# Kernel optimization log

Hardware: AMD Instinct MI355X
Metric: run time of the kernel (lower is better)

## Reference

```python
import jax, jax.numpy as jnp
import numpy as np

NB = 8          # num_bins
HID = 128       # hidden channels of coupling ResidualNet
TB = 3.0        # tail_bound
MINB = 1e-3     # min bin width / height
MIND = 1e-3     # min derivative
DCONST = float(np.log(np.exp(1.0 - MIND) - 1.0))  # softplus(DCONST)+MIND == 1
LU_EPS = 1e-3


def rqs_inverse(x, uw, uh, ud):
    """Inverse monotonic rational-quadratic spline with linear tails (nflows math).
    x: [B,F]; uw,uh broadcastable to [B,F,NB]; ud broadcastable to [B,F,NB-1]."""
    K = NB
    uw = jnp.broadcast_to(uw, x.shape + (K,))
    uh = jnp.broadcast_to(uh, x.shape + (K,))
    ud = jnp.broadcast_to(ud, x.shape + (K - 1,))
    ud = jnp.pad(ud, [(0, 0)] * x.ndim + [(1, 1)], constant_values=DCONST)  # boundary derivs = 1
    inside = (x >= -TB) & (x <= TB)
    xi = jnp.clip(x, -TB, TB)

    def knots(u):
        v = MINB + (1.0 - MINB * K) * jax.nn.softmax(u, -1)
        c = jnp.concatenate([jnp.zeros(x.shape + (1,), x.dtype), jnp.cumsum(v, -1)], -1)
        c = 2.0 * TB * c - TB
        c = c.at[..., 0].set(-TB).at[..., -1].set(TB)
        return c, c[..., 1:] - c[..., :-1]

    cw, w = knots(uw)   # x-knots / bin widths
    ch, h = knots(uh)   # y-knots / bin heights
    d = MIND + jax.nn.softplus(ud)  # [B,F,K+1] knot derivatives

    # searchsorted on cumheights (inverse direction)
    locs = ch.at[..., -1].add(1e-6)
    idx = jnp.clip(jnp.sum((xi[..., None] >= locs).astype(jnp.int32), -1) - 1, 0, K - 1)[..., None]
    g = lambda a: jnp.take_along_axis(a, idx, -1)[..., 0]
    in_cw, in_w, in_ch, in_h = g(cw), g(w), g(ch), g(h)
    delta = in_h / in_w
    d0 = g(d)
    d1 = jnp.take_along_axis(d, idx + 1, -1)[..., 0]

    t = xi - in_ch
    s = d0 + d1 - 2.0 * delta
    a = t * s + in_h * (delta - d0)
    b = in_h * d0 - t * s
    c = -delta * t
    root = (2.0 * c) / (-b - jnp.sqrt(b * b - 4.0 * a * c))
    out = root * in_w + in_cw
    tm = root * (1.0 - root)
    den = delta + s * tm
    dnum = delta ** 2 * (d1 * root ** 2 + 2.0 * delta * tm + d0 * (1.0 - root) ** 2)
    ld = -(jnp.log(dnum) - 2.0 * jnp.log(den))
    return jnp.where(inside, out, x), jnp.where(inside, ld, 0.0)


def resnet(x, Wi, bi, Wb, bb, Wo, bo):
    # nflows ResidualNet: initial linear, 2 pre-activation residual blocks, final linear
    t = x @ Wi + bi
    for j in range(2):
        r = jax.nn.relu(t) @ Wb[2 * j] + bb[2 * j]
        r = jax.nn.relu(r) @ Wb[2 * j + 1] + bb[2 * j + 1]
        t = t + r
    return t @ Wo + bo


def coupling_inverse(z, Wi, bi, Wb, bb, Wo, bo, uw_u, uh_u, ud_u):
    # alternating mask: even dims = identity split, odd dims = transform split
    ident, trans = z[:, 0::2], z[:, 1::2]
    # unconditional spline on identity features is inverted FIRST, then feeds the net
    ident, ld_u = rqs_inverse(ident, uw_u, uh_u, ud_u)
    B, F = trans.shape
    p = resnet(ident, Wi, bi, Wb, bb, Wo, bo).reshape(B, F, 3 * NB - 1)
    scale = 1.0 / np.sqrt(HID)  # nflows divides widths/heights by sqrt(hidden_features)
    trans, ld_t = rqs_inverse(trans, p[..., :NB] * scale, p[..., NB:2 * NB] * scale, p[..., 2 * NB:])
    out = jnp.stack([ident, trans], -1).reshape(B, -1)
    return out, jnp.sum(ld_u, -1) + jnp.sum(ld_t, -1)


def log_prob(x, loc, log_scale, Wi, bi, Wb, bb, Wo, bo, uw_u, uh_u, ud_u,
             lu_lower, lu_upper, lu_ud, lu_b, perms):
    N, T, D = x.shape
    z = x.reshape(-1, D)
    lq = jnp.zeros((z.shape[0],), x.dtype)
    for i in (2, 1, 0):  # flows = [C0,LU0,C1,LU1,C2,LU2]; invert in reverse order
        # LULinearPermute.inverse: permute, then y = L(Ux) + b, logdet = sum log diag(U)
        zp = z[:, perms[i]]
        diag = jax.nn.softplus(lu_ud[i]) + LU_EPS
        U = jnp.triu(lu_upper[i], 1) + jnp.diag(diag)
        L = jnp.tril(lu_lower[i], -1) + jnp.eye(D, dtype=x.dtype)
        z = (zp @ U.T) @ L.T + lu_b[i]
        lq = lq + jnp.sum(jnp.log(diag))
        z, ld = coupling_inverse(z, Wi[i], bi[i], Wb[i], bb[i], Wo[i], bo[i],
                                 uw_u[i], uh_u[i], ud_u[i])
        lq = lq + ld
    # DiagGaussian base log-prob
    lq = lq - 0.5 * D * jnp.log(2.0 * jnp.pi) \
            - jnp.sum(log_scale + 0.5 * ((z - loc) / jnp.exp(log_scale)) ** 2, -1)
    return lq.reshape(N, T)


def setup_inputs():
    key = jax.random.key(0)
    ks = jax.random.split(key, 16)
    N, T, D, F = 8, 512, 550, 275
    OUT = F * (3 * NB - 1)
    s = 0.1
    return {
        "x": jax.random.normal(ks[0], (N, T, D), jnp.float32),
        "loc": 0.1 * jax.random.normal(ks[1], (D,), jnp.float32),
        "log_scale": jnp.zeros((D,), jnp.float32),
        "Wi": s * jax.random.normal(ks[2], (3, F, HID), jnp.float32),
        "bi": jnp.zeros((3, HID), jnp.float32),
        "Wb": s * jax.random.normal(ks[3], (3, 4, HID, HID), jnp.float32),
        "bb": jnp.zeros((3, 4, HID), jnp.float32),
        "Wo": 0.01 * jax.random.normal(ks[4], (3, HID, OUT), jnp.float32),
        "bo": 0.01 * jax.random.normal(ks[5], (3, OUT), jnp.float32),
        "uw_u": jax.random.uniform(ks[6], (3, F, NB), jnp.float32),
        "uh_u": jax.random.uniform(ks[7], (3, F, NB), jnp.float32),
        "ud_u": jax.random.uniform(ks[8], (3, F, NB - 1), jnp.float32),
        "lu_lower": 0.05 * jax.random.normal(ks[9], (3, D, D), jnp.float32),
        "lu_upper": 0.05 * jax.random.normal(ks[10], (3, D, D), jnp.float32),
        "lu_ud": jnp.full((3, D), DCONST, jnp.float32),
        "lu_b": jnp.zeros((3, D), jnp.float32),
        "perms": jnp.stack([jax.random.permutation(ks[11 + i], D) for i in range(3)]).astype(jnp.int32),
    }


def reference(x, loc, log_scale, Wi, bi, Wb, bb, Wo, bo, uw_u, uh_u, ud_u,
              lu_lower, lu_upper, lu_ud, lu_b, perms):
    # log_prob(x).reshape(N, T); calculate_likelihood would just apply exp/nan->0/clamp on top.
    return log_prob(x, loc, log_scale, Wi, bi, Wb, bb, Wo, bo, uw_u, uh_u, ud_u,
                    lu_lower, lu_upper, lu_ud, lu_b, perms)
```

## Files before the change

### kernel.cpp

```cpp
#include <hip/hip_runtime.h>


#define D_DIM 550
#define D_PAD 576
#define N_PAD_A 640
#define F_DIM 275
#define F_PAD 320
#define FP_HALF 288
#define HID_DIM 128
#define OUT_DIM 6325
#define OUT_PAD 6400
#define FT_PAD 276
#define WO2_ROWS (FT_PAD*32)
#define WO_GX (WO2_ROWS/128)
#define B_ROWS 4096
#define NBINS 8
#define TB_C 3.0f
#define MINB_C 0.001f
#define MIND_C 0.001f
#define DCONST_C 0.53974233f
#define LUEPS_C 0.001f
#define RSQRT_HID 0.08838834764831845f

typedef unsigned short ushort_t;
typedef __attribute__((ext_vector_type(8))) short short8;
typedef __attribute__((ext_vector_type(8))) unsigned short ushort8;
typedef __attribute__((ext_vector_type(4))) unsigned short ushort4v;
typedef __attribute__((ext_vector_type(4))) float f32x4;

__device__ __forceinline__ ushort_t f2bf(float f){
    union{float f; unsigned u;} v; v.f = f;
    unsigned r = v.u + 0x7fffu + ((v.u>>16)&1u);
    return (ushort_t)(r>>16);
}
__device__ __forceinline__ float bf2f(ushort_t h){
    union{unsigned u; float f;} v; v.u = ((unsigned)h)<<16;
    return v.f;
}
__device__ __forceinline__ float softplusf(float x){
    return fmaxf(x, 0.f) + __logf(1.f + __expf(-fabsf(x)));
}

__device__ __forceinline__ void knots_from_u(const float* u, float* c, float* w){
    float m = u[0];
#pragma unroll
    for(int k=1;k<NBINS;k++) m = fmaxf(m, u[k]);
    float e[NBINS]; float s = 0.f;
#pragma unroll
    for(int k=0;k<NBINS;k++){ e[k] = __expf(u[k]-m); s += e[k]; }
    float inv = 1.f/s;
    float cum = 0.f;
    c[0] = -TB_C;
#pragma unroll
    for(int k=0;k<NBINS;k++){
        float v = MINB_C + (1.f - MINB_C*(float)NBINS)*e[k]*inv;
        cum += v;
        c[k+1] = 2.f*TB_C*cum - TB_C;
    }
    c[NBINS] = TB_C;
#pragma unroll
    for(int k=0;k<NBINS;k++) w[k] = c[k+1]-c[k];
}

__device__ __forceinline__ void rqs_inv(float x,
                                        const float* cw, const float* w,
                                        const float* ch, const float* h,
                                        const float* d,
                                        float& out, float& ld){
    bool inside = (x >= -TB_C) && (x <= TB_C);
    float xi = fminf(fmaxf(x, -TB_C), TB_C);
    int idx = 0;
#pragma unroll
    for(int j=1;j<NBINS;j++) idx += (xi >= ch[j]) ? 1 : 0;
    float icw=cw[0], iw=w[0], ich=ch[0], ih=h[0], d0=d[0], d1=d[1];
#pragma unroll
    for(int j=1;j<NBINS;j++){
        if(idx==j){ icw=cw[j]; iw=w[j]; ich=ch[j]; ih=h[j]; d0=d[j]; d1=d[j+1]; }
    }
    float delta = ih/iw;
    float t  = xi - ich;
    float s  = d0 + d1 - 2.f*delta;
    float a  = t*s + ih*(delta - d0);
    float b  = ih*d0 - t*s;
    float c  = -delta*t;
    float disc = b*b - 4.f*a*c;
    float root = 2.f*c / (-b - sqrtf(fmaxf(disc, 0.f)));
    float o  = root*iw + icw;
    float tm = root*(1.f-root);
    float den  = delta + s*tm;
    float dnum = delta*delta*(d1*root*root + 2.f*delta*tm + d0*(1.f-root)*(1.f-root));
    float l = 2.f*__logf(den) - __logf(dnum);
    out = inside ? o : x;
    ld  = inside ? l : 0.f;
}


__global__ void build_knots_kernel(const float* __restrict__ uw_u,
                                   const float* __restrict__ uh_u,
                                   const float* __restrict__ ud_u,
                                   float* __restrict__ knots){
    int g = blockIdx.x*blockDim.x + threadIdx.x;
    if(g >= 3*F_DIM) return;
    float* kb = knots + (size_t)g*43;
    float c[9], w[8];
    knots_from_u(uw_u + (size_t)g*8, c, w);
#pragma unroll
    for(int k=0;k<9;k++) kb[k]=c[k];
#pragma unroll
    for(int k=0;k<8;k++) kb[9+k]=w[k];
    knots_from_u(uh_u + (size_t)g*8, c, w);
#pragma unroll
    for(int k=0;k<9;k++) kb[17+k]=c[k];
#pragma unroll
    for(int k=0;k<8;k++) kb[26+k]=w[k];
    float dend = MIND_C + softplusf(DCONST_C);
    kb[34]=dend; kb[42]=dend;
    const float* ud = ud_u + (size_t)g*7;
#pragma unroll
    for(int k=0;k<7;k++) kb[35+k] = MIND_C + softplusf(ud[k]);
}

__global__ void logdiag_kernel(const float* __restrict__ lu_ud, float* __restrict__ outv){
    int tid = threadIdx.x;
    float s = 0.f;
    for(int k=tid; k<3*D_DIM; k+=256) s += __logf(softplusf(lu_ud[k]) + LUEPS_C);
#pragma unroll
    for(int o=32;o>0;o>>=1) s += __shfl_down(s, o);
    __shared__ float sm[4];
    if((tid&63)==0) sm[tid>>6]=s;
    __syncthreads();
    if(tid==0) outv[0] = sm[0]+sm[1]+sm[2]+sm[3];
}

__global__ void build_L_bf16(const float* __restrict__ lower,
                             ushort_t* __restrict__ Lmb){
    int l = blockIdx.z;
    lower += (size_t)l*D_DIM*D_DIM;
    Lmb += (size_t)l*N_PAD_A*D_PAD;
    int k = blockIdx.x*blockDim.x + threadIdx.x;
    int j = blockIdx.y;
    if(k >= D_DIM) return;
    float lv = (j>k) ? lower[(size_t)j*D_DIM+k] : (j==k ? 1.f : 0.f);
    Lmb[(size_t)j*D_PAD+k] = f2bf(lv);
}

__global__ void build_UT_bf16(const float* __restrict__ upper,
                              const float* __restrict__ ud,
                              const int* __restrict__ perm,
                              ushort_t* __restrict__ UpTb){
    int l = blockIdx.z;
    upper += (size_t)l*D_DIM*D_DIM; ud += (size_t)l*D_DIM; perm += (size_t)l*D_DIM;
    UpTb += (size_t)l*N_PAD_A*D_PAD;
    __shared__ float t[32][33];
    int j0 = blockIdx.x*32, k0 = blockIdx.y*32;
    int tx = threadIdx.x, ty = threadIdx.y;
#pragma unroll
    for(int i=0;i<32;i+=8){
        int j = j0+ty+i, k = k0+tx;
        float uv = 0.f;
        if(j<D_DIM && k<D_DIM){
            if(j<k)       uv = upper[(size_t)j*D_DIM+k];
            else if(j==k) uv = softplusf(ud[k]) + LUEPS_C;
        }
        t[ty+i][tx] = uv;
    }
    __syncthreads();
#pragma unroll
    for(int i=0;i<32;i+=8){
        int k = k0+ty+i, j = j0+tx;
        if(k<D_DIM)
            UpTb[(size_t)perm[k]*D_PAD + j] = f2bf(t[tx][ty+i]);
    }
}

__global__ void convert_pad(const float* __restrict__ in, ushort_t* __restrict__ out,
                            int M, int K, int Mpad, int Kpad){
    int idx = blockIdx.x*256 + threadIdx.x;
    if(idx >= Mpad*Kpad) return;
    int r = idx / Kpad, c = idx - r*Kpad;
    float v = (r<M && c<K) ? in[(size_t)r*K+c] : 0.f;
    out[idx] = f2bf(v);
}

template<int REMAP>
__global__ void transpose_convert(const float* __restrict__ in, ushort_t* __restrict__ out,
                                  int K, int N, int Kpad, int Npad, long s_in, long s_out){
    in += (size_t)blockIdx.z*s_in; out += (size_t)blockIdx.z*s_out;
    __shared__ float t[32][33];
    int kb = blockIdx.x*32, nb = blockIdx.y*32;
    int tx = threadIdx.x, ty = threadIdx.y;
#pragma unroll
    for(int i=0;i<32;i+=8){
        int k = kb+ty+i, n = nb+tx;
        t[ty+i][tx] = (k<K && n<N) ? in[(size_t)k*N+n] : 0.f;
    }
    __syncthreads();
#pragma unroll
    for(int i=0;i<32;i+=8){
        int n = nb+ty+i, k = kb+tx;
        if(REMAP){
            if(n < OUT_DIM && k < Kpad){
                int f = n/23, j = n - 23*f;
                out[(size_t)(f*32+j)*Kpad+k] = f2bf(t[tx][ty+i]);
            }
        } else if(n<Npad && k<Kpad){
            out[(size_t)n*Kpad+k] = f2bf(t[tx][ty+i]);
        }
    }
}

__global__ void reorder_bias(const float* __restrict__ bo, float* __restrict__ bo2){
    int idx = blockIdx.x*256 + threadIdx.x;
    if(idx >= 3*OUT_DIM) return;
    int l = idx/OUT_DIM, n = idx%OUT_DIM;
    int f = n/23, j = n - 23*f;
    bo2[(size_t)l*WO2_ROWS + f*32 + j] = bo[idx];
}

template<int OUTBF>
__global__ __launch_bounds__(256)
void gemm_mfma(const ushort_t* __restrict__ A, const ushort_t* __restrict__ Bt,
               const float* __restrict__ bias, void* __restrict__ Cv,
               int M, int N, int Kpad, long sA, long sB, long sC){
    A  += (size_t)blockIdx.z*sA;
    Bt += (size_t)blockIdx.z*sB;
    __shared__ ushort_t As[128][72];
    __shared__ ushort_t Bs[128][72];
    int tid = threadIdx.x;
    int row0 = blockIdx.y*128, col0 = blockIdx.x*128;
    int wave = tid>>6, lane = tid&63;
    int wm = wave&1, wn = wave>>1;
    int lm = lane&15, quad = lane>>4;
    f32x4 acc[4][4] = {};
    for(int k0=0; k0<Kpad; k0+=64){
#pragma unroll
        for(int it=0; it<4; it++){
            int c = tid + it*256;
            int r = c>>3, c8 = (c&7)*8;
            *(ushort8*)&As[r][c8] = *(const ushort8*)(A + (size_t)(row0+r)*Kpad + k0 + c8);
            *(ushort8*)&Bs[r][c8] = *(const ushort8*)(Bt + (size_t)(col0+r)*Kpad + k0 + c8);
        }
        __syncthreads();
#pragma unroll
        for(int ks=0; ks<2; ks++){
            short8 af[4], bfr[4];
#pragma unroll
            for(int i=0;i<4;i++){
                af[i]  = *(const short8*)&As[wm*64 + i*16 + lm][ks*32 + quad*8];
                bfr[i] = *(const short8*)&Bs[wn*64 + i*16 + lm][ks*32 + quad*8];
            }
#pragma unroll
            for(int i=0;i<4;i++)
#pragma unroll
                for(int j=0;j<4;j++)
                    acc[i][j] = __builtin_amdgcn_mfma_f32_16x16x32_bf16(af[i], bfr[j], acc[i][j], 0, 0, 0);
        }
        __syncthreads();
    }
#pragma unroll
    for(int i=0;i<4;i++){
        int rbase = row0 + wm*64 + i*16 + quad*4;
#pragma unroll
        for(int j=0;j<4;j++){
            int gc = col0 + wn*64 + j*16 + lm;
            if(gc >= N) continue;
            float bv = bias[gc];
#pragma unroll
            for(int r=0;r<4;r++){
                int gr = rbase + r;
                float v = acc[i][j][r] + bv;
                if(OUTBF) ((ushort_t*)Cv + (size_t)blockIdx.z*sC)[(size_t)gr*N+gc] = f2bf(v);
                else      ((float*)Cv + (size_t)blockIdx.z*sC)[(size_t)gr*N+gc] = v;
            }
        }
    }
}

__global__ __launch_bounds__(256)
void resnet_fused(const ushort_t* __restrict__ identb,
                  const ushort_t* __restrict__ WiT,
                  const float* __restrict__ bi,
                  const ushort_t* __restrict__ WbT,
                  const float* __restrict__ bb,
                  ushort_t* __restrict__ tb){
    __shared__ ushort_t As2[16][136];
    int tid = threadIdx.x, wave = tid>>6, lane = tid&63;
    int lm = lane&15, quad = lane>>4;
    int r0 = blockIdx.x*16;
    int arow = r0 + lm;
    f32x4 cur[2] = {};
    f32x4 tsv[2];
    for(int k0=0; k0<F_PAD; k0+=64){
        const ushort_t* ap = identb + (size_t)arow*F_PAD + k0 + quad*8;
        short8 af0 = *(const short8*)(ap);
        short8 af1 = *(const short8*)(ap + 32);
#pragma unroll
        for(int jj=0;jj<2;jj++){
            int n = (wave*2+jj)*16 + lm;
            const ushort_t* wp = WiT + (size_t)n*F_PAD + k0 + quad*8;
            short8 b0 = *(const short8*)(wp);
            short8 b1 = *(const short8*)(wp + 32);
            cur[jj] = __builtin_amdgcn_mfma_f32_16x16x32_bf16(af0, b0, cur[jj], 0, 0, 0);
            cur[jj] = __builtin_amdgcn_mfma_f32_16x16x32_bf16(af1, b1, cur[jj], 0, 0, 0);
        }
    }
#pragma unroll
    for(int jj=0;jj<2;jj++){
        float bv = bi[(wave*2+jj)*16 + lm];
#pragma unroll
        for(int r=0;r<4;r++) cur[jj][r] += bv;
        tsv[jj] = cur[jj];
    }
    short8 wA[2][4], wB[2][4];
#pragma unroll
    for(int jj=0;jj<2;jj++){
        int n = (wave*2+jj)*16 + lm;
        const ushort_t* wp = WbT + (size_t)n*128 + quad*8;
#pragma unroll
        for(int ks=0;ks<4;ks++) wA[jj][ks] = *(const short8*)(wp + ks*32);
    }
#pragma unroll
    for(int st=0; st<4; st++){
        __syncthreads();
#pragma unroll
        for(int jj=0;jj<2;jj++)
#pragma unroll
            for(int r=0;r<4;r++)
                As2[quad*4 + r][(wave*2+jj)*16 + lm] = f2bf(fmaxf(cur[jj][r], 0.f));
        if(st < 3){
#pragma unroll
            for(int jj=0;jj<2;jj++){
                int n = (wave*2+jj)*16 + lm;
                const ushort_t* wp = WbT + (size_t)(st+1)*128*128 + (size_t)n*128 + quad*8;
#pragma unroll
                for(int ks=0;ks<4;ks++){
                    if(st & 1) wA[jj][ks] = *(const short8*)(wp + ks*32);
                    else       wB[jj][ks] = *(const short8*)(wp + ks*32);
                }
            }
        }
        __syncthreads();
        short8 af[4];
#pragma unroll
        for(int ks=0;ks<4;ks++) af[ks] = *(const short8*)&As2[lm][ks*32 + quad*8];
        f32x4 acc[2] = {};
#pragma unroll
        for(int ks=0;ks<4;ks++){
#pragma unroll
            for(int jj=0;jj<2;jj++){
                short8 bf = (st & 1) ? wB[jj][ks] : wA[jj][ks];
                acc[jj] = __builtin_amdgcn_mfma_f32_16x16x32_bf16(af[ks], bf, acc[jj], 0, 0, 0);
            }
        }
#pragma unroll
        for(int jj=0;jj<2;jj++){
            float bv = bb[st*128 + (wave*2+jj)*16 + lm];
#pragma unroll
            for(int r=0;r<4;r++) acc[jj][r] += bv;
        }
        if(st==1 || st==3){
#pragma unroll
            for(int jj=0;jj<2;jj++){
#pragma unroll
                for(int r=0;r<4;r++) acc[jj][r] += tsv[jj][r];
                tsv[jj] = acc[jj];
            }
        }
#pragma unroll
        for(int jj=0;jj<2;jj++) cur[jj] = acc[jj];
    }
#pragma unroll
    for(int jj=0;jj<2;jj++)
#pragma unroll
        for(int r=0;r<4;r++)
            tb[(size_t)(r0 + quad*4 + r)*HID_DIM + (wave*2+jj)*16 + lm] = f2bf(cur[jj][r]);
}

__global__ __launch_bounds__(256)
void zodd_transpose(const float* __restrict__ z2, float* __restrict__ z2oddT){
    __shared__ float s[32][65];
    int r0 = blockIdx.x*64, f0 = blockIdx.y*32;
    int tid = threadIdx.x;
    int f = tid & 31, rb = tid >> 5;
#pragma unroll
    for(int rr=0; rr<8; rr++){
        int r = rb + rr*8;
        int fg = f0 + f;
        float v = (fg < F_DIM) ? z2[(size_t)(r0+r)*D_DIM + 2*fg + 1] : 0.f;
        s[f][r] = v;
    }
    __syncthreads();
    int lane = tid & 63, fb = tid >> 6;
#pragma unroll
    for(int ff=0; ff<8; ff++){
        int fo = fb + ff*4;
        z2oddT[(size_t)(f0+fo)*B_ROWS + r0 + lane] = s[fo][lane];
    }
}

__global__ __launch_bounds__(256, 2)
void wo_spline(const ushort_t* __restrict__ tb,
               const ushort_t* __restrict__ Wo2,
               const float* __restrict__ bo2,
               const float* __restrict__ z2oddT,
               ushort_t* __restrict__ zOddT,
               float* __restrict__ ldpart){
    __shared__ __align__(16) char smem[128*133*4];
    __shared__ float ldred[128];
    ushort_t (*As)[72] = (ushort_t(*)[72])smem;
    ushort_t (*Bs)[72] = (ushort_t(*)[72])(smem + 128*72*2);
    float (*P)[133] = (float(*)[133])smem;
    int tid = threadIdx.x;
    int flat = blockIdx.y*WO_GX + blockIdx.x;
    int flat2 = (flat & 7)*(WO_GX*32/8) + (flat >> 3);
    int cbl = flat2 % WO_GX;
    int rbl = flat2 / WO_GX;
    int row0 = rbl*128, col0 = cbl*128;
    int wave = tid>>6, lane = tid&63;
    int wm = wave&1, wn = wave>>1;
    int lm = lane&15, quad = lane>>4;
    f32x4 acc[4][4] = {};
    for(int k0=0; k0<HID_DIM; k0+=64){
#pragma unroll
        for(int it=0; it<4; it++){
            int c = tid + it*256;
            int r = c>>3, c8 = (c&7)*8;
            *(ushort8*)&As[r][c8] = *(const ushort8*)(tb + (size_t)(row0+r)*HID_DIM + k0 + c8);
            *(ushort8*)&Bs[r][c8] = *(const ushort8*)(Wo2 + (size_t)(col0+r)*HID_DIM + k0 + c8);
        }
        __syncthreads();
#pragma unroll
        for(int ks=0; ks<2; ks++){
            short8 af[4], bfr[4];
#pragma unroll
            for(int i=0;i<4;i++){
                af[i]  = *(const short8*)&As[wm*64 + i*16 + lm][ks*32 + quad*8];
                bfr[i] = *(const short8*)&Bs[wn*64 + i*16 + lm][ks*32 + quad*8];
            }
#pragma unroll
            for(int i=0;i<4;i++)
#pragma unroll
                for(int j=0;j<4;j++)
                    acc[i][j] = __builtin_amdgcn_mfma_f32_16x16x32_bf16(af[i], bfr[j], acc[i][j], 0, 0, 0);
        }
        __syncthreads();
    }
#pragma unroll
    for(int j=0;j<4;j++){
        int cl = wn*64 + j*16 + lm;
        float bv = bo2[col0 + cl];
#pragma unroll
        for(int i=0;i<4;i++){
            int rl = wm*64 + i*16 + quad*4;
#pragma unroll
            for(int r=0;r<4;r++) P[rl+r][cl] = acc[i][j][r] + bv;
        }
    }
    __syncthreads();
    int row = tid & 127;
    int fbase = col0 >> 5;
    float ldsum = 0.f;
    const float dend = MIND_C + softplusf(DCONST_C);
#pragma unroll
    for(int e2=0;e2<2;e2++){
        int feat = (tid>>7) + e2*2;
        int fg = fbase + feat;
        if(fg < F_DIM){
            const float* q = &P[row][feat*32];
            float xv = z2oddT[(size_t)fg*B_ROWS + row0 + row];
            bool inside = (xv >= -TB_C) && (xv <= TB_C);
            float xi = fminf(fmaxf(xv, -TB_C), TB_C);
            float eh[8];
            float mh = -1e30f, sh = 0.f;
#pragma unroll
            for(int k=0;k<8;k++){ float u = q[8+k]*RSQRT_HID; eh[k]=u; mh=fmaxf(mh,u); }
#pragma unroll
            for(int k=0;k<8;k++){ eh[k] = __expf(eh[k]-mh); sh += eh[k]; }
            float invh = (1.f - MINB_C*8.f)/sh;
            int idx = 0;
            {
                float cum = 0.f;
#pragma unroll
                for(int k=0;k<7;k++){
                    cum += MINB_C + eh[k]*invh;
                    float ck = 2.f*TB_C*cum - TB_C;
                    idx += (xi >= ck) ? 1 : 0;
                }
            }
            float ich = -TB_C, ihh = 0.f;
            {
                float cum = 0.f, cprev = -TB_C;
#pragma unroll
                for(int k=0;k<8;k++){
                    cum += MINB_C + eh[k]*invh;
                    float ck = (k==7) ? TB_C : (2.f*TB_C*cum - TB_C);
                    if(idx==k){ ich = cprev; ihh = ck - cprev; }
                    cprev = ck;
                }
            }
            float ew[8];
            float mw = -1e30f, sw = 0.f;
#pragma unroll
            for(int k=0;k<8;k++){ float u = q[k]*RSQRT_HID; ew[k]=u; mw=fmaxf(mw,u); }
#pragma unroll
            for(int k=0;k<8;k++){ ew[k] = __expf(ew[k]-mw); sw += ew[k]; }
            float invw = (1.f - MINB_C*8.f)/sw;
            float icw = -TB_C, iww = 0.f;
            {
                float cum = 0.f, cprev = -TB_C;
#pragma unroll
                for(int k=0;k<8;k++){
                    cum += MINB_C + ew[k]*invw;
                    float ck = (k==7) ? TB_C : (2.f*TB_C*cum - TB_C);
                    if(idx==k){ icw = cprev; iww = ck - cprev; }
                    cprev = ck;
                }
            }
            float d0 = (idx==0) ? dend : (MIND_C + softplusf(q[15+idx]));
            float d1 = (idx==7) ? dend : (MIND_C + softplusf(q[16+idx]));
            float delta = ihh/iww;
            float t  = xi - ich;
            float s  = d0 + d1 - 2.f*delta;
            float a  = t*s + ihh*(delta - d0);
            float b  = ihh*d0 - t*s;
            float c  = -delta*t;
            float disc = fmaxf(b*b - 4.f*a*c, 0.f);
            float root = 2.f*c / (-b - sqrtf(disc));
            float o  = root*iww + icw;
            float tm = root*(1.f-root);
            float den  = delta + s*tm;
            float dnum = delta*delta*(d1*root*root + 2.f*delta*tm + d0*(1.f-root)*(1.f-root));
            float l = 2.f*__logf(den) - __logf(dnum);
            zOddT[(size_t)fg*B_ROWS + row0 + row] = f2bf(inside ? o : xv);
            ldsum += inside ? l : 0.f;
        }
    }
    if(tid >= 128) ldred[tid-128] = ldsum;
    __syncthreads();
    if(tid < 128) ldpart[(size_t)cbl*B_ROWS + row0 + tid] = ldsum + ldred[tid];
}

__global__ __launch_bounds__(256)
void interleave_z(const ushort_t* __restrict__ identb,
                  const ushort_t* __restrict__ zOddT,
                  const float* __restrict__ ldpart,
                  ushort_t* __restrict__ znb,
                  float* __restrict__ lq){
    __shared__ ushort_t s[FP_HALF][34];
    int r0 = blockIdx.x*32;
    int tid = threadIdx.x;
#pragma unroll
    for(int i=0;i<36;i++){
        int idx = tid + i*256;
        int f = idx>>5, r = idx&31;
        s[f][r] = zOddT[(size_t)f*B_ROWS + r0 + r];
    }
    __syncthreads();
    int wv = tid>>6, lane = tid&63;
#pragma unroll
    for(int k=0;k<8;k++){
        int r = wv + k*4;
        const ushort_t* idr = identb + (size_t)(r0+r)*F_PAD;
        unsigned* orow = (unsigned*)(znb + (size_t)(r0+r)*D_PAD);
#pragma unroll
        for(int c=0;c<5;c++){
            int f = lane + c*64;
            if(f < FP_HALF){
                unsigned lo = idr[f];
                unsigned hi = s[f][r];
                orow[f] = lo | (hi<<16);
            }
        }
    }
    if(tid < 32){
        float acc = 0.f;
        for(int cb=0; cb<WO_GX; cb++)
            acc += ldpart[(size_t)cb*B_ROWS + r0 + tid];
        lq[r0 + tid] += acc;
    }
}


__global__ __launch_bounds__(320)
void ident_spline_kernel(const float* __restrict__ z2, const float* __restrict__ knots,
                         int layer, ushort_t* __restrict__ identb,
                         float* __restrict__ lq){
    int row = blockIdx.x; int tid = threadIdx.x;
    float ldv = 0.f;
    if(tid < F_DIM){
        const float* kb = knots + ((size_t)(layer*F_DIM + tid))*43;
        float x = z2[(size_t)row*D_DIM + 2*tid];
        float o, l;
        rqs_inv(x, kb, kb+9, kb+17, kb+26, kb+34, o, l);
        identb[(size_t)row*F_PAD + tid] = f2bf(o);
        ldv = l;
    } else {
        identb[(size_t)row*F_PAD + tid] = 0;
    }
    __shared__ float sm[5];
    float v = ldv;
#pragma unroll
    for(int o=32;o>0;o>>=1) v += __shfl_down(v, o);
    if((tid&63)==0) sm[tid>>6]=v;
    __syncthreads();
    if(tid==0) lq[row] += sm[0]+sm[1]+sm[2]+sm[3]+sm[4];
}

__global__ __launch_bounds__(320)
void finalize_kernel(const ushort_t* __restrict__ zb, const float* __restrict__ loc,
                     const float* __restrict__ lsc, const float* __restrict__ lq,
                     const float* __restrict__ logdiag, float* __restrict__ out){
    int row = blockIdx.x; int tid = threadIdx.x;
    float s = 0.f;
    for(int k=tid; k<D_DIM; k+=320){
        float l = lsc[k];
        float diff = (bf2f(zb[(size_t)row*D_PAD+k])-loc[k])*__expf(-l);
        s += l + 0.5f*diff*diff;
    }
    __shared__ float sm[5];
#pragma unroll
    for(int o=32;o>0;o>>=1) s += __shfl_down(s, o);
    if((tid&63)==0) sm[tid>>6]=s;
    __syncthreads();
    if(tid==0){
        float tot = sm[0]+sm[1]+sm[2]+sm[3]+sm[4];
        out[row] = lq[row] + logdiag[0] - 275.f*1.8378770664f - tot;
    }
}


extern "C" void kernel_launch(void* const* d_in, const int* in_sizes, int n_in,
                              void* d_out, int out_size, void* d_ws, size_t ws_size,
                              hipStream_t stream){
    const float* x        = (const float*)d_in[0];
    const float* loc      = (const float*)d_in[1];
    const float* lsc      = (const float*)d_in[2];
    const float* Wi       = (const float*)d_in[3];
    const float* bi       = (const float*)d_in[4];
    const float* Wb       = (const float*)d_in[5];
    const float* bb       = (const float*)d_in[6];
    const float* Wo       = (const float*)d_in[7];
    const float* bo       = (const float*)d_in[8];
    const float* uw_u     = (const float*)d_in[9];
    const float* uh_u     = (const float*)d_in[10];
    const float* ud_u     = (const float*)d_in[11];
    const float* lu_lower = (const float*)d_in[12];
    const float* lu_upper = (const float*)d_in[13];
    const float* lu_ud    = (const float*)d_in[14];
    const float* lu_b     = (const float*)d_in[15];
    const int*   perms    = (const int*)d_in[16];
    float* out = (float*)d_out;

    char* base = (char*)d_ws;
    size_t off = 0;
    auto alloc = [&](size_t bytes)->char*{
        char* p = base + off;
        off += (bytes + 255) & ~(size_t)255;
        return p;
    };
    float* lq      = (float*)alloc(B_ROWS*4);
    float* zbias   = (float*)alloc(D_PAD*4);
    float* logdiag = (float*)alloc(64*4);
    float* knots   = (float*)alloc((size_t)3*F_DIM*43*4);
    float* z2      = (float*)alloc((size_t)B_ROWS*D_DIM*4);
    float* z2oddT  = (float*)alloc((size_t)FP_HALF*B_ROWS*4);
    float* ldpart  = (float*)alloc((size_t)WO_GX*B_ROWS*4);
    float* bo2     = (float*)alloc((size_t)3*WO2_ROWS*4);
    ushort_t* xb   = (ushort_t*)alloc((size_t)B_ROWS*D_PAD*2);
    ushort_t* zbf0 = (ushort_t*)alloc((size_t)B_ROWS*D_PAD*2);
    ushort_t* zbf1 = (ushort_t*)alloc((size_t)B_ROWS*D_PAD*2);
    ushort_t* zOddT= (ushort_t*)alloc((size_t)FP_HALF*B_ROWS*2);
    ushort_t* Lmb  = (ushort_t*)alloc((size_t)3*N_PAD_A*D_PAD*2);
    ushort_t* UpTb = (ushort_t*)alloc((size_t)3*N_PAD_A*D_PAD*2);
    ushort_t* Apb  = (ushort_t*)alloc((size_t)3*N_PAD_A*D_PAD*2);
    ushort_t* identb=(ushort_t*)alloc((size_t)B_ROWS*F_PAD*2);
    ushort_t* tb   = (ushort_t*)alloc((size_t)B_ROWS*HID_DIM*2);
    ushort_t* WiT  = (ushort_t*)alloc((size_t)3*HID_DIM*F_PAD*2);
    ushort_t* WbT  = (ushort_t*)alloc((size_t)3*4*HID_DIM*HID_DIM*2);
    ushort_t* Wo2  = (ushort_t*)alloc((size_t)3*WO2_ROWS*HID_DIM*2);

    hipMemsetAsync(lq, 0, B_ROWS*sizeof(float), stream);
    hipMemsetAsync(zbias, 0, D_PAD*sizeof(float), stream);
    hipMemsetAsync(zOddT, 0, (size_t)FP_HALF*B_ROWS*2, stream);
    hipMemsetAsync(Lmb, 0, (size_t)3*N_PAD_A*D_PAD*2, stream);
    hipMemsetAsync(UpTb, 0, (size_t)3*N_PAD_A*D_PAD*2, stream);
    hipMemsetAsync(Wo2, 0, (size_t)3*WO2_ROWS*HID_DIM*2, stream);
    hipMemsetAsync(bo2, 0, (size_t)3*WO2_ROWS*4, stream);
    build_knots_kernel<<<dim3((3*F_DIM+255)/256), dim3(256), 0, stream>>>(uw_u, uh_u, ud_u, knots);
    logdiag_kernel<<<dim3(1), dim3(256), 0, stream>>>(lu_ud, logdiag);
    convert_pad<<<dim3((B_ROWS*D_PAD+255)/256), dim3(256), 0, stream>>>(
        x, xb, B_ROWS, D_DIM, B_ROWS, D_PAD);
    build_L_bf16<<<dim3((D_DIM+255)/256, D_DIM, 3), dim3(256), 0, stream>>>(
        lu_lower, Lmb);
    dim3 tthr(32,8);
    build_UT_bf16<<<dim3(18, 18, 3), tthr, 0, stream>>>(
        lu_upper, lu_ud, perms, UpTb);
    gemm_mfma<1><<<dim3(5, 5, 3), dim3(256), 0, stream>>>(
        Lmb, UpTb, zbias, Apb, N_PAD_A, D_PAD, D_PAD,
        (long)N_PAD_A*D_PAD, (long)N_PAD_A*D_PAD, (long)N_PAD_A*D_PAD);
    transpose_convert<0><<<dim3(F_PAD/32, HID_DIM/32, 3), tthr, 0, stream>>>(
        Wi, WiT, F_DIM, HID_DIM, F_PAD, HID_DIM, (long)F_DIM*HID_DIM, (long)F_PAD*HID_DIM);
    transpose_convert<0><<<dim3(HID_DIM/32, HID_DIM/32, 12), tthr, 0, stream>>>(
        Wb, WbT, HID_DIM, HID_DIM, HID_DIM, HID_DIM, (long)HID_DIM*HID_DIM, (long)HID_DIM*HID_DIM);
    transpose_convert<1><<<dim3(HID_DIM/32, OUT_PAD/32, 3), tthr, 0, stream>>>(
        Wo, Wo2, HID_DIM, OUT_DIM, HID_DIM, OUT_PAD, (long)HID_DIM*OUT_DIM, (long)WO2_ROWS*HID_DIM);
    reorder_bias<<<dim3((3*OUT_DIM+255)/256), dim3(256), 0, stream>>>(bo, bo2);

    const ushort_t* zcur_b = xb;
    ushort_t* zbf[2] = {zbf0, zbf1};
    int zi = 0;

    for(int it=0; it<3; ++it){
        int i = 2 - it;

        gemm_mfma<0><<<dim3(N_PAD_A/128, B_ROWS/128), dim3(256), 0, stream>>>(
            zcur_b, Apb + (size_t)i*N_PAD_A*D_PAD, lu_b + (size_t)i*D_DIM,
            z2, B_ROWS, D_DIM, D_PAD, 0, 0, 0);

        zodd_transpose<<<dim3(B_ROWS/64, FP_HALF/32), dim3(256), 0, stream>>>(
            z2, z2oddT);

        ident_spline_kernel<<<dim3(B_ROWS), dim3(320), 0, stream>>>(
            z2, knots, i, identb, lq);

        resnet_fused<<<dim3(B_ROWS/16), dim3(256), 0, stream>>>(
            identb, WiT + (size_t)i*HID_DIM*F_PAD, bi + (size_t)i*HID_DIM,
            WbT + (size_t)i*4*HID_DIM*HID_DIM, bb + (size_t)i*4*HID_DIM, tb);

        wo_spline<<<dim3(WO_GX, B_ROWS/128), dim3(256), 0, stream>>>(
            tb, Wo2 + (size_t)i*WO2_ROWS*HID_DIM, bo2 + (size_t)i*WO2_ROWS,
            z2oddT, zOddT, ldpart);

        interleave_z<<<dim3(B_ROWS/32), dim3(256), 0, stream>>>(
            identb, zOddT, ldpart, zbf[zi], lq);

        zcur_b = zbf[zi];
        zi ^= 1;
    }

    finalize_kernel<<<dim3(B_ROWS), dim3(320), 0, stream>>>(
        zcur_b, loc, lsc, lq, logdiag, out);
}
```

Baseline: 428.7 us.

## Fuse LU GEMM with identity-half spline, odd transpose and bf16 packing

```diff
diff --git a/kernel.cpp b/kernel.cpp
--- a/kernel.cpp
+++ b/kernel.cpp
@@ -13,6 +13,7 @@
 #define FT_PAD 276
 #define WO2_ROWS (FT_PAD*32)
 #define WO_GX (WO2_ROWS/128)
+#define GI_GX 5
 #define B_ROWS 4096
 #define NBINS 8
 #define TB_C 3.0f
@@ -25,7 +26,6 @@
 typedef unsigned short ushort_t;
 typedef __attribute__((ext_vector_type(8))) short short8;
 typedef __attribute__((ext_vector_type(8))) unsigned short ushort8;
-typedef __attribute__((ext_vector_type(4))) unsigned short ushort4v;
 typedef __attribute__((ext_vector_type(4))) float f32x4;
 
 __device__ __forceinline__ ushort_t f2bf(float f){
@@ -273,6 +273,96 @@
                 else      ((float*)Cv + (size_t)blockIdx.z*sC)[(size_t)gr*N+gc] = v;
             }
         }
+    }
+}
+
+__global__ __launch_bounds__(256, 2)
+void gemm_ident_spline(const ushort_t* __restrict__ A,
+                       const ushort_t* __restrict__ Bt,
+                       const float* __restrict__ bias,
+                       const float* __restrict__ knots,
+                       ushort_t* __restrict__ identb,
+                       float* __restrict__ z2oddT,
+                       float* __restrict__ ldpartI){
+    __shared__ __align__(16) char smem[128*133*4];
+    __shared__ float ldred[128];
+    ushort_t (*As)[72] = (ushort_t(*)[72])smem;
+    ushort_t (*Bs)[72] = (ushort_t(*)[72])(smem + 128*72*2);
+    float (*P)[133] = (float(*)[133])smem;
+    int tid = threadIdx.x;
+    int flat = blockIdx.y*GI_GX + blockIdx.x;
+    int flat2 = (flat & 7)*20 + (flat >> 3);
+    int cbl = flat2 % GI_GX;
+    int rbl = flat2 / GI_GX;
+    int row0 = rbl*128, col0 = cbl*128;
+    int wave = tid>>6, lane = tid&63;
+    int wm = wave&1, wn = wave>>1;
+    int lm = lane&15, quad = lane>>4;
+    f32x4 acc[4][4] = {};
+    for(int k0=0; k0<D_PAD; k0+=64){
+#pragma unroll
+        for(int it=0; it<4; it++){
+            int c = tid + it*256;
+            int r = c>>3, c8 = (c&7)*8;
+            *(ushort8*)&As[r][c8] = *(const ushort8*)(A + (size_t)(row0+r)*D_PAD + k0 + c8);
+            *(ushort8*)&Bs[r][c8] = *(const ushort8*)(Bt + (size_t)(col0+r)*D_PAD + k0 + c8);
+        }
+        __syncthreads();
+#pragma unroll
+        for(int ks=0; ks<2; ks++){
+            short8 af[4], bfr[4];
+#pragma unroll
+            for(int i=0;i<4;i++){
+                af[i]  = *(const short8*)&As[wm*64 + i*16 + lm][ks*32 + quad*8];
+                bfr[i] = *(const short8*)&Bs[wn*64 + i*16 + lm][ks*32 + quad*8];
+            }
+#pragma unroll
+            for(int i=0;i<4;i++)
+#pragma unroll
+                for(int j=0;j<4;j++)
+                    acc[i][j] = __builtin_amdgcn_mfma_f32_16x16x32_bf16(af[i], bfr[j], acc[i][j], 0, 0, 0);
+        }
+        __syncthreads();
+    }
+#pragma unroll
+    for(int j=0;j<4;j++){
+        int cl = wn*64 + j*16 + lm;
+        int gc = col0 + cl;
+        float bv = (gc < D_DIM) ? bias[gc] : 0.f;
+#pragma unroll
+        for(int i=0;i<4;i++){
+            int rl = wm*64 + i*16 + quad*4;
+#pragma unroll
+            for(int r=0;r<4;r++) P[rl+r][cl] = acc[i][j][r] + bv;
+        }
+    }
+    __syncthreads();
+    int row = tid & 127, half = tid >> 7;
+    float ldsum = 0.f;
+    for(int fl=0; fl<32; fl++){
+        int fgl = half*32 + fl;
+        int fg  = cbl*64 + fgl;
+        float xe = P[row][2*fgl];
+        float o = 0.f, l = 0.f;
+        if(fg < F_DIM){
+            const float* kb = knots + (size_t)fg*43;
+            rqs_inv(xe, kb, kb+9, kb+17, kb+26, kb+34, o, l);
+            z2oddT[(size_t)fg*B_ROWS + row0 + row] = P[row][2*fgl+1];
+        }
+        P[row][2*fgl] = o;
+        ldsum += l;
+    }
+    if(half) ldred[row] = ldsum;
+    __syncthreads();
+    if(tid < 128) ldpartI[(size_t)cbl*B_ROWS + row0 + tid] = ldsum + ldred[tid];
+    unsigned* id32 = (unsigned*)identb;
+#pragma unroll
+    for(int rep=0; rep<16; rep++){
+        int idx = tid + rep*256;
+        int r = idx >> 5, ui = idx & 31;
+        unsigned lo = f2bf(P[r][4*ui]);
+        unsigned hi = f2bf(P[r][4*ui+2]);
+        id32[(size_t)(row0+r)*(F_PAD/2) + cbl*32 + ui] = lo | (hi<<16);
     }
 }
 
@@ -374,28 +464,6 @@
 #pragma unroll
         for(int r=0;r<4;r++)
             tb[(size_t)(r0 + quad*4 + r)*HID_DIM + (wave*2+jj)*16 + lm] = f2bf(cur[jj][r]);
-}
-
-__global__ __launch_bounds__(256)
-void zodd_transpose(const float* __restrict__ z2, float* __restrict__ z2oddT){
-    __shared__ float s[32][65];
-    int r0 = blockIdx.x*64, f0 = blockIdx.y*32;
-    int tid = threadIdx.x;
-    int f = tid & 31, rb = tid >> 5;
-#pragma unroll
-    for(int rr=0; rr<8; rr++){
-        int r = rb + rr*8;
-        int fg = f0 + f;
-        float v = (fg < F_DIM) ? z2[(size_t)(r0+r)*D_DIM + 2*fg + 1] : 0.f;
-        s[f][r] = v;
-    }
-    __syncthreads();
-    int lane = tid & 63, fb = tid >> 6;
-#pragma unroll
-    for(int ff=0; ff<8; ff++){
-        int fo = fb + ff*4;
-        z2oddT[(size_t)(f0+fo)*B_ROWS + r0 + lane] = s[fo][lane];
-    }
 }
 
 __global__ __launch_bounds__(256, 2)
@@ -544,6 +612,7 @@
 void interleave_z(const ushort_t* __restrict__ identb,
                   const ushort_t* __restrict__ zOddT,
                   const float* __restrict__ ldpart,
+                  const float* __restrict__ ldpartI,
                   ushort_t* __restrict__ znb,
                   float* __restrict__ lq){
     __shared__ ushort_t s[FP_HALF][34];
@@ -576,35 +645,12 @@
         float acc = 0.f;
         for(int cb=0; cb<WO_GX; cb++)
             acc += ldpart[(size_t)cb*B_ROWS + r0 + tid];
+        for(int cb=0; cb<GI_GX; cb++)
+            acc += ldpartI[(size_t)cb*B_ROWS + r0 + tid];
         lq[r0 + tid] += acc;
     }
 }
 
-
-__global__ __launch_bounds__(320)
-void ident_spline_kernel(const float* __restrict__ z2, const float* __restrict__ knots,
-                         int layer, ushort_t* __restrict__ identb,
-                         float* __restrict__ lq){
-    int row = blockIdx.x; int tid = threadIdx.x;
-    float ldv = 0.f;
-    if(tid < F_DIM){
-        const float* kb = knots + ((size_t)(layer*F_DIM + tid))*43;
-        float x = z2[(size_t)row*D_DIM + 2*tid];
-        float o, l;
-        rqs_inv(x, kb, kb+9, kb+17, kb+26, kb+34, o, l);
-        identb[(size_t)row*F_PAD + tid] = f2bf(o);
-        ldv = l;
-    } else {
-        identb[(size_t)row*F_PAD + tid] = 0;
-    }
-    __shared__ float sm[5];
-    float v = ldv;
-#pragma unroll
-    for(int o=32;o>0;o>>=1) v += __shfl_down(v, o);
-    if((tid&63)==0) sm[tid>>6]=v;
-    __syncthreads();
-    if(tid==0) lq[row] += sm[0]+sm[1]+sm[2]+sm[3]+sm[4];
-}
 
 __global__ __launch_bounds__(320)
 void finalize_kernel(const ushort_t* __restrict__ zb, const float* __restrict__ loc,
@@ -662,9 +708,9 @@
     float* zbias   = (float*)alloc(D_PAD*4);
     float* logdiag = (float*)alloc(64*4);
     float* knots   = (float*)alloc((size_t)3*F_DIM*43*4);
-    float* z2      = (float*)alloc((size_t)B_ROWS*D_DIM*4);
     float* z2oddT  = (float*)alloc((size_t)FP_HALF*B_ROWS*4);
     float* ldpart  = (float*)alloc((size_t)WO_GX*B_ROWS*4);
+    float* ldpartI = (float*)alloc((size_t)GI_GX*B_ROWS*4);
     float* bo2     = (float*)alloc((size_t)3*WO2_ROWS*4);
     ushort_t* xb   = (ushort_t*)alloc((size_t)B_ROWS*D_PAD*2);
     ushort_t* zbf0 = (ushort_t*)alloc((size_t)B_ROWS*D_PAD*2);
@@ -713,15 +759,9 @@
     for(int it=0; it<3; ++it){
         int i = 2 - it;
 
-        gemm_mfma<0><<<dim3(N_PAD_A/128, B_ROWS/128), dim3(256), 0, stream>>>(
+        gemm_ident_spline<<<dim3(GI_GX, B_ROWS/128), dim3(256), 0, stream>>>(
             zcur_b, Apb + (size_t)i*N_PAD_A*D_PAD, lu_b + (size_t)i*D_DIM,
-            z2, B_ROWS, D_DIM, D_PAD, 0, 0, 0);
-
-        zodd_transpose<<<dim3(B_ROWS/64, FP_HALF/32), dim3(256), 0, stream>>>(
-            z2, z2oddT);
-
-        ident_spline_kernel<<<dim3(B_ROWS), dim3(320), 0, stream>>>(
-            z2, knots, i, identb, lq);
+            knots + (size_t)i*F_DIM*43, identb, z2oddT, ldpartI);
 
         resnet_fused<<<dim3(B_ROWS/16), dim3(256), 0, stream>>>(
             identb, WiT + (size_t)i*HID_DIM*F_PAD, bi + (size_t)i*HID_DIM,
@@ -732,7 +772,7 @@
             z2oddT, zOddT, ldpart);
 
         interleave_z<<<dim3(B_ROWS/32), dim3(256), 0, stream>>>(
-            identb, zOddT, ldpart, zbf[zi], lq);
+            identb, zOddT, ldpart, ldpartI, zbf[zi], lq);
 
         zcur_b = zbf[zi];
         zi ^= 1;
```

Result: slower. 441.4 us (+2.9%).
